# Optimization experiments

Hardware: AMD Instinct MI355X
Metric: run time of the kernel (lower is better)

## Reference

```python
import jax, jax.numpy as jnp
import numpy as np
from jax import lax

# program token ids
PAD, START, END, SCENE, INTERSECT, FILT, RELATE, QUERY = range(8)
SKIP = (PAD, START, END)


def conv2d(x, w, b, dil=1):
    # 'same' padding for odd kernels (3x3 pad=dil, 1x1 pad=0), NCHW/OIHW
    pad = dil * (w.shape[2] // 2)
    y = lax.conv_general_dilated(x, w, (1, 1), [(pad, pad), (pad, pad)],
                                 rhs_dilation=(dil, dil),
                                 dimension_numbers=('NCHW', 'OIHW', 'NCHW'))
    return y + b[None, :, None, None]


def maxpool2(x):
    return lax.reduce_window(x, -jnp.inf, lax.max, (1, 1, 2, 2), (1, 1, 2, 2), 'VALID')


def exec_program(prog, feat_input, p):
    """Run one (concrete) program over a batch of stem features. prog: tuple of ints,
    executed in reversed order exactly like TbDNet.forward."""
    B, _, H, W = feat_input.shape
    output = feat_input
    saved = None
    for t in reversed(prog):
        if t in SKIP:
            continue
        if t == SCENE:
            saved = output
            output = jnp.ones((B, 1, H, W), feat_input.dtype)
        elif t == INTERSECT:  # AndModule: elementwise min of attentions
            output = jnp.minimum(output, saved)
        elif t == FILT:
            a = feat_input * output  # [B,D,H,W] * [B,1,H,W]
            a = jax.nn.relu(conv2d(a, p['att_w1'], p['att_b1']))
            a = jax.nn.relu(conv2d(a, p['att_w2'], p['att_b2']))
            output = jax.nn.sigmoid(conv2d(a, p['att_w3'], p['att_b3']))
        elif t == RELATE:  # RelateModule: dilated conv stack (1,2,4,8,1) -> conv1x1 sigmoid
            a = feat_input * output
            for w, b, d in ((p['rel_w1'], p['rel_b1'], 1), (p['rel_w2'], p['rel_b2'], 2),
                            (p['rel_w3'], p['rel_b3'], 4), (p['rel_w4'], p['rel_b4'], 8),
                            (p['rel_w5'], p['rel_b5'], 1)):
                a = jax.nn.relu(conv2d(a, w, b, d))
            output = jax.nn.sigmoid(conv2d(a, p['rel_w6'], p['rel_b6']))
        elif t == QUERY:
            a = feat_input * output
            a = jax.nn.relu(conv2d(a, p['qry_w1'], p['qry_b1']))
            output = jax.nn.relu(conv2d(a, p['qry_w2'], p['qry_b2']))
    return output


def tbd_forward(feats, programs_np, p):
    B = feats.shape[0]
    stem = jax.nn.relu(conv2d(feats, p['stem_w1'], p['stem_b1']))
    stem = jax.nn.relu(conv2d(stem, p['stem_w2'], p['stem_b2']))  # [B,D,H,W]
    D, H, W = stem.shape[1], stem.shape[2], stem.shape[3]
    # group samples by identical program so dispatch runs batched, not per-sample
    groups = {}
    for n in range(B):
        groups.setdefault(tuple(int(v) for v in programs_np[n]), []).append(n)
    mod_out = jnp.zeros((B, D, H, W), feats.dtype)
    for prog, idxs in groups.items():
        idx = jnp.array(idxs)
        mod_out = mod_out.at[idx].set(exec_program(prog, stem[idx], p))
    # classifier: conv1x1 -> relu -> maxpool2 -> flatten -> fc -> relu -> fc
    x = jax.nn.relu(conv2d(mod_out, p['cls_w'], p['cls_b']))
    x = maxpool2(x)                        # [B,1024,7,7]
    x = x.reshape(B, -1)                   # [B,50176]
    x = jax.nn.relu(x @ p['fc1_w'].T + p['fc1_b'])
    return x @ p['fc2_w'].T + p['fc2_b']   # [B,28]


def setup_inputs() -> dict:
    key = jax.random.key(0)
    ks = iter(jax.random.split(key, 64))
    def rn(shape, s=0.05):
        return jax.random.normal(next(ks), shape, dtype=jnp.float32) * s
    B, Cin, H, W, D, P, L, A = 64, 1024, 14, 14, 128, 1024, 1024, 28
    feats = jax.random.normal(next(ks), (B, Cin, H, W), dtype=jnp.float32)
    # stored programs; execution order is reversed(stored)
    progA = [START, QUERY, FILT, RELATE, FILT, SCENE, END, PAD]            # scene->filter->relate->filter->query
    progB = [START, QUERY, INTERSECT, FILT, SCENE, FILT, SCENE, END]       # two filter branches -> intersect -> query
    programs = jnp.array([progA] * (B // 2) + [progB] * (B // 2), dtype=jnp.int32)
    inp = {'feats': feats, 'programs': programs,
           'stem_w1': rn((D, Cin, 3, 3), 0.02), 'stem_b1': rn((D,)),
           'stem_w2': rn((D, D, 3, 3)), 'stem_b2': rn((D,)),
           'att_w1': rn((D, D, 3, 3)), 'att_b1': rn((D,)),
           'att_w2': rn((D, D, 3, 3)), 'att_b2': rn((D,)),
           'att_w3': rn((1, D, 1, 1)), 'att_b3': rn((1,)),
           'rel_w1': rn((D, D, 3, 3)), 'rel_b1': rn((D,)),
           'rel_w2': rn((D, D, 3, 3)), 'rel_b2': rn((D,)),
           'rel_w3': rn((D, D, 3, 3)), 'rel_b3': rn((D,)),
           'rel_w4': rn((D, D, 3, 3)), 'rel_b4': rn((D,)),
           'rel_w5': rn((D, D, 3, 3)), 'rel_b5': rn((D,)),
           'rel_w6': rn((1, D, 1, 1)), 'rel_b6': rn((1,)),
           'qry_w1': rn((D, D, 3, 3)), 'qry_b1': rn((D,)),
           'qry_w2': rn((D, D, 3, 3)), 'qry_b2': rn((D,)),
           'cls_w': rn((P, D, 1, 1)), 'cls_b': rn((P,)),
           'fc1_w': rn((L, P * (H // 2) * (W // 2)), 0.01), 'fc1_b': rn((L,)),
           'fc2_w': rn((A, L)), 'fc2_b': rn((A,))}
    return inp


PARAM_NAMES = ['stem_w1', 'stem_b1', 'stem_w2', 'stem_b2',
               'att_w1', 'att_b1', 'att_w2', 'att_b2', 'att_w3', 'att_b3',
               'rel_w1', 'rel_b1', 'rel_w2', 'rel_b2', 'rel_w3', 'rel_b3',
               'rel_w4', 'rel_b4', 'rel_w5', 'rel_b5', 'rel_w6', 'rel_b6',
               'qry_w1', 'qry_b1', 'qry_w2', 'qry_b2',
               'cls_w', 'cls_b', 'fc1_w', 'fc1_b', 'fc2_w', 'fc2_b']


def reference(feats, programs, stem_w1, stem_b1, stem_w2, stem_b2,
              att_w1, att_b1, att_w2, att_b2, att_w3, att_b3,
              rel_w1, rel_b1, rel_w2, rel_b2, rel_w3, rel_b3,
              rel_w4, rel_b4, rel_w5, rel_b5, rel_w6, rel_b6,
              qry_w1, qry_b1, qry_w2, qry_b2,
              cls_w, cls_b, fc1_w, fc1_b, fc2_w, fc2_b):
    vals = [stem_w1, stem_b1, stem_w2, stem_b2,
            att_w1, att_b1, att_w2, att_b2, att_w3, att_b3,
            rel_w1, rel_b1, rel_w2, rel_b2, rel_w3, rel_b3,
            rel_w4, rel_b4, rel_w5, rel_b5, rel_w6, rel_b6,
            qry_w1, qry_b1, qry_w2, qry_b2,
            cls_w, cls_b, fc1_w, fc1_b, fc2_w, fc2_b]
    p = dict(zip(PARAM_NAMES, vals))
    return tbd_forward(feats, np.asarray(programs), p)
```

## Files before the change

kernel.cpp:

```cpp
#include <hip/hip_runtime.h>
#include <math.h>


typedef __attribute__((ext_vector_type(8)))  short   short8;
typedef __attribute__((ext_vector_type(8)))  __bf16  bf16x8;
typedef __attribute__((ext_vector_type(4)))  float   f32x4;

#define NROUNDS 15
#define NKS 49

#define B_WSTEM1 0UL
#define B_WSTEM2 2359296UL
#define B_WMOD   2654208UL
#define B_WCLS   5308416UL
#define B_STEM   5570560UL
#define B_XA     8781824UL
#define B_XB     11993088UL
#define B_FEAT   15204352UL
#define B_ATTN   18415616UL
#define B_SAVED  18465792UL
#define B_SCHED  18515968UL
#define B_ACTB   18520064UL
#define B_FC1T   24942592UL
#define B_S1P    B_XB
#define B_FC1P   B_STEM

__device__ __forceinline__ unsigned short f2bf(float f) {
    unsigned int b = __float_as_uint(f);
    b += 0x7fffu + ((b >> 16) & 1u);
    return (unsigned short)(b >> 16);
}
__device__ __forceinline__ float bf2f(unsigned short u) {
    return __uint_as_float(((unsigned int)u) << 16);
}
__device__ __forceinline__ f32x4 mfma16(bf16x8 a, bf16x8 b, f32x4 c) {
    return __builtin_amdgcn_mfma_f32_16x16x32_bf16(a, b, c, 0, 0, 0);
}

struct RepackArgs { const float* src[12]; };

__global__ __launch_bounds__(256) void k_repack(RepackArgs a, char* ws)
{
    const int y = blockIdx.y;
    const float* __restrict__ src = a.src[y];
    int gid = blockIdx.x * 256 + threadIdx.x;
    int gsz = gridDim.x * 256;
    if (y == 11) {
        unsigned short* dst = (unsigned short*)(ws + B_WCLS);
        for (int i = gid; i < 131072; i += gsz) dst[i] = f2bf(src[i]);
    } else {
        const int IC = (y == 0) ? 1024 : 128;
        const int lg = (y == 0) ? 10 : 7;
        unsigned short* dst = (unsigned short*)(ws + ((y == 0) ? B_WSTEM1
                                    : (y == 1) ? B_WSTEM2
                                    : B_WMOD + (size_t)(y - 2) * 294912));
        const int total = 9 << (lg + 7);
        for (int i = gid; i < total; i += gsz) {
            int ic = i & (IC - 1);
            int oc = (i >> lg) & 127;
            int t  = i >> (lg + 7);
            dst[i] = f2bf(src[((size_t)oc * IC + ic) * 9 + t]);
        }
    }
}

__global__ __launch_bounds__(256) void k_decode_init(const int* __restrict__ prog, char* ws)
{
    int gid = blockIdx.x * 256 + threadIdx.x;
    int gsz = gridDim.x * 256;
    float* attn  = (float*)(ws + B_ATTN);
    float* saved = (float*)(ws + B_SAVED);
    for (int i = gid; i < 64 * 196; i += gsz) { attn[i] = 1.0f; saved[i] = 1.0f; }
    unsigned int* fz = (unsigned int*)(ws + B_FEAT);
    for (int i = gid; i < 64 * 25088 / 2; i += gsz) fz[i] = 0u;
    if (gid < 64) {
        int n = gid;
        int ent[NROUNDS];
        for (int r = 0; r < NROUNDS; ++r) ent[r] = 0;
        int rc = 0;
#define ENC(op,wv,dl,g,s,d) ((op)|((wv)<<4)|((dl)<<8)|((g)<<12)|((s)<<13)|((d)<<15))
#define EMIT(v) do { if (rc < NROUNDS) ent[rc++] = (v); } while (0)
        for (int j = 7; j >= 0; --j) {
            int t = prog[n * 8 + j];
            switch (t) {
                case 3: EMIT(ENC(1,0,0,0,0,0)); break;
                case 4: EMIT(ENC(2,0,0,0,0,0)); break;
                case 5:
                    EMIT(ENC(3,0,1,1,3,0));
                    EMIT(ENC(3,1,1,0,0,1));
                    EMIT(ENC(4,0,0,0,1,0));
                    break;
                case 6:
                    EMIT(ENC(3,2,1,1,3,0));
                    EMIT(ENC(3,3,2,0,0,1));
                    EMIT(ENC(3,4,4,0,1,0));
                    EMIT(ENC(3,5,8,0,0,1));
                    EMIT(ENC(3,6,1,0,1,0));
                    EMIT(ENC(4,1,0,0,0,0));
                    break;
                case 7:
                    EMIT(ENC(3,7,1,1,3,0));
                    EMIT(ENC(3,8,1,0,0,2));
                    break;
                default: break;
            }
        }
#undef EMIT
#undef ENC
        int* sched = (int*)(ws + B_SCHED);
        for (int r = 0; r < NROUNDS; ++r) sched[n * NROUNDS + r] = ent[r];
    }
}

__global__ __launch_bounds__(256) void k_stem1p(const float* __restrict__ feats,
                                                const unsigned short* __restrict__ wrep,
                                                char* ws)
{
    __shared__ unsigned short s_img[197 * 136];
    const int bx = blockIdx.x;
    const int n = bx >> 4, ks = (bx >> 2) & 3, och = (bx >> 1) & 1, pxh = bx & 1;
    const int tid = threadIdx.x, lane = tid & 63;
    const int w = tid >> 6, wm = w & 1, wn = w >> 1;
    const int l15 = lane & 15, lq = lane >> 4;

    if (tid < 68) ((unsigned int*)s_img)[196 * 68 + tid] = 0u;

    int pglob[4], pbyt[4], pyv[4], pxv[4];
#pragma unroll
    for (int j = 0; j < 4; ++j) {
        int nt = wn + 2 * j;
        int p  = (pxh * 7 + nt) * 16 + l15;
        pglob[j] = p;
        int py = p / 14;
        pyv[j] = (p < 196) ? py : 10000;
        pxv[j] = p - py * 14;
        pbyt[j] = p * 272 + lq * 16;
    }
    const int zaddr = 196 * 272 + lq * 16;
    const int nNT = (wn == 0) ? 4 : 3;

    f32x4 acc[2][4];
#pragma unroll
    for (int m = 0; m < 2; ++m)
#pragma unroll
        for (int j = 0; j < 4; ++j) acc[m][j] = (f32x4){0.f, 0.f, 0.f, 0.f};

    const int icg = tid & 31;

    for (int slab = 0; slab < 2; ++slab) {
        if (slab) __syncthreads();
        const int icb = ks * 256 + slab * 128;
        const float* sf = feats + ((size_t)n * 1024 + icb) * 196;
        for (int qq = (tid >> 5); qq < 49; qq += 8) {
            const float* p0 = sf + icg * 4 * 196 + qq * 4;
            float4 r0 = *(const float4*)(p0);
            float4 r1 = *(const float4*)(p0 + 196);
            float4 r2 = *(const float4*)(p0 + 392);
            float4 r3 = *(const float4*)(p0 + 588);
#pragma unroll
            for (int e = 0; e < 4; ++e) {
                uint2 v;
                v.x = (unsigned int)f2bf(((const float*)&r0)[e]) |
                      ((unsigned int)f2bf(((const float*)&r1)[e]) << 16);
                v.y = (unsigned int)f2bf(((const float*)&r2)[e]) |
                      ((unsigned int)f2bf(((const float*)&r3)[e]) << 16);
                *(uint2*)(s_img + (qq * 4 + e) * 136 + icg * 4) = v;
            }
        }
        __syncthreads();

#pragma unroll
        for (int t = 0; t < 9; ++t) {
            const int dy = t / 3 - 1, dx = t % 3 - 1;
            int baddr[4];
#pragma unroll
            for (int j = 0; j < 4; ++j) {
                int yy = pyv[j] + dy, xx = pxv[j] + dx;
                bool ok = ((unsigned)yy < 14u) && ((unsigned)xx < 14u);
                baddr[j] = ok ? (pbyt[j] + (dy * 14 + dx) * 272) : zaddr;
            }
#pragma unroll
            for (int kc = 0; kc < 4; ++kc) {
                const unsigned short* wt = wrep +
                    ((size_t)(t * 128 + och * 64 + wm * 32 + l15) * 1024 + icb + kc * 32 + lq * 8);
                bf16x8 a0 = *(const bf16x8*)(wt);
                bf16x8 a1 = *(const bf16x8*)(wt + 16 * 1024);
#pragma unroll
                for (int j = 0; j < 4; ++j) {
                    if (j < nNT) {
                        bf16x8 b = *(const bf16x8*)((const char*)s_img + baddr[j] + kc * 64);
                        acc[0][j] = mfma16(a0, b, acc[0][j]);
                        acc[1][j] = mfma16(a1, b, acc[1][j]);
                    }
                }
            }
        }
    }

    unsigned short* part = (unsigned short*)(ws + B_S1P);
#pragma unroll
    for (int m = 0; m < 2; ++m) {
        const int oc = och * 64 + wm * 32 + m * 16 + lq * 4;
#pragma unroll
        for (int j = 0; j < 4; ++j) {
            if (j < nNT) {
                int p = pglob[j];
                if (p < 196) {
                    unsigned int lo = (unsigned int)f2bf(acc[m][j][0]) |
                                      ((unsigned int)f2bf(acc[m][j][1]) << 16);
                    unsigned int hi = (unsigned int)f2bf(acc[m][j][2]) |
                                      ((unsigned int)f2bf(acc[m][j][3]) << 16);
                    uint2 pk; pk.x = lo; pk.y = hi;
                    *(uint2*)(part + (((size_t)ks * 64 + n) * 196 + p) * 128 + oc) = pk;
                }
            }
        }
    }
}

__global__ __launch_bounds__(256) void k_stem1r(const char* __restrict__ ws_c,
                                                const float* __restrict__ bias,
                                                unsigned short* __restrict__ xa)
{
    int i = blockIdx.x * 256 + threadIdx.x;
    const unsigned short* part = (const unsigned short*)(ws_c + B_S1P);
    int oc8 = (i & 15) * 8;
    int np  = i >> 4;
    float s[8] = {};
#pragma unroll
    for (int ks = 0; ks < 4; ++ks) {
        short8 v = *(const short8*)(part + (((size_t)ks * 64) * 196 + np) * 128 + oc8);
#pragma unroll
        for (int e = 0; e < 8; ++e) s[e] += bf2f((unsigned short)v[e]);
    }
    short8 o;
#pragma unroll
    for (int e = 0; e < 8; ++e)
        o[e] = (short)f2bf(fmaxf(s[e] + bias[oc8 + e], 0.f));
    *(short8*)(xa + (size_t)np * 128 + oc8) = o;
}

__device__ void conv_mfma_core(const unsigned short* __restrict__ srcB,
                               const float*  __restrict__ gate,
                               const unsigned short* __restrict__ wrep,
                               const float*  __restrict__ bias,
                               unsigned short* __restrict__ dst,
                               int dil, int och, int pxh,
                               unsigned short* s_img)
{
    const int tid  = threadIdx.x, lane = tid & 63;
    const int w    = tid >> 6, wm = w & 1, wn = w >> 1;
    const int l15  = lane & 15, lq = lane >> 4;

    if (tid < 68) ((unsigned int*)s_img)[196 * 68 + tid] = 0u;

    int pglob[4], pbyt[4], pyv[4], pxv[4];
#pragma unroll
    for (int j = 0; j < 4; ++j) {
        int nt = wn + 2 * j;
        int p  = (pxh * 7 + nt) * 16 + l15;
        pglob[j] = p;
        int py = p / 14;
        pyv[j] = (p < 196) ? py : 10000;
        pxv[j] = p - py * 14;
        pbyt[j] = p * 272 + lq * 16;
    }
    const int zaddr = 196 * 272 + lq * 16;
    const int nNT = (wn == 0) ? 4 : 3;

    f32x4 acc[2][4];
#pragma unroll
    for (int m = 0; m < 2; ++m)
#pragma unroll
        for (int j = 0; j < 4; ++j) acc[m][j] = (f32x4){0.f, 0.f, 0.f, 0.f};

    if (gate) {
        for (int i = tid; i < 196 * 16; i += 256) {
            int p = i >> 4, c8 = (i & 15) * 8;
            short8 v = *(const short8*)(srcB + p * 128 + c8);
            float g = gate[p];
            short8 ov;
#pragma unroll
            for (int e = 0; e < 8; ++e)
                ov[e] = (short)f2bf(bf2f((unsigned short)v[e]) * g);
            *(short8*)(s_img + p * 136 + c8) = ov;
        }
    } else {
        for (int i = tid; i < 196 * 16; i += 256) {
            int p = i >> 4, c8 = (i & 15) * 8;
            *(short8*)(s_img + p * 136 + c8) = *(const short8*)(srcB + p * 128 + c8);
        }
    }
    __syncthreads();

    const unsigned short* wlane = wrep + (size_t)(och * 64 + wm * 32 + l15) * 128 + lq * 8;
#pragma unroll
    for (int t = 0; t < 9; ++t) {
        const int dy = (t / 3 - 1) * dil, dx = (t % 3 - 1) * dil;
        int baddr[4];
#pragma unroll
        for (int j = 0; j < 4; ++j) {
            int yy = pyv[j] + dy, xx = pxv[j] + dx;
            bool ok = ((unsigned)yy < 14u) && ((unsigned)xx < 14u);
            baddr[j] = ok ? (pbyt[j] + (dy * 14 + dx) * 272) : zaddr;
        }
        const unsigned short* wt = wlane + (size_t)(t * 128) * 128;
#pragma unroll
        for (int kc = 0; kc < 4; ++kc) {
            bf16x8 a0 = *(const bf16x8*)(wt + kc * 32);
            bf16x8 a1 = *(const bf16x8*)(wt + (size_t)16 * 128 + kc * 32);
#pragma unroll
            for (int j = 0; j < 4; ++j) {
                if (j < nNT) {
                    bf16x8 b = *(const bf16x8*)((const char*)s_img + baddr[j] + kc * 64);
                    acc[0][j] = mfma16(a0, b, acc[0][j]);
                    acc[1][j] = mfma16(a1, b, acc[1][j]);
                }
            }
        }
    }

#pragma unroll
    for (int m = 0; m < 2; ++m) {
        const int oc = och * 64 + wm * 32 + m * 16 + lq * 4;
        const float4 b4 = *(const float4*)(bias + oc);
#pragma unroll
        for (int j = 0; j < 4; ++j) {
            if (j < nNT) {
                int p = pglob[j];
                if (p < 196) {
                    float v0 = fmaxf(acc[m][j][0] + b4.x, 0.f);
                    float v1 = fmaxf(acc[m][j][1] + b4.y, 0.f);
                    float v2 = fmaxf(acc[m][j][2] + b4.z, 0.f);
                    float v3 = fmaxf(acc[m][j][3] + b4.w, 0.f);
                    unsigned int lo = (unsigned int)f2bf(v0) | ((unsigned int)f2bf(v1) << 16);
                    unsigned int hi = (unsigned int)f2bf(v2) | ((unsigned int)f2bf(v3) << 16);
                    uint2 pk; pk.x = lo; pk.y = hi;
                    *(uint2*)(dst + p * 128 + oc) = pk;
                }
            }
        }
    }
}

__global__ __launch_bounds__(256) void k_conv_stem2(const unsigned short* __restrict__ srcBall,
                                                    const unsigned short* __restrict__ wrep,
                                                    const float* __restrict__ bias,
                                                    unsigned short* __restrict__ dstall)
{
    __shared__ unsigned short s_img[197 * 136];
    const int n = blockIdx.x >> 2, och = (blockIdx.x >> 1) & 1, pxh = blockIdx.x & 1;
    conv_mfma_core(srcBall + (size_t)n * 25088, nullptr, wrep, bias,
                   dstall + (size_t)n * 25088, 1, och, pxh, s_img);
}

struct RArgs {
    char* ws;
    const float* mbias[9];
    const float* w1x1[2];
    const float* b1x1[2];
};

__global__ __launch_bounds__(256) void k_round(RArgs a, int r)
{
    __shared__ unsigned short s_img[197 * 136];
    const int bx = blockIdx.x;
    const int n = bx >> 2, och = (bx >> 1) & 1, pxh = bx & 1;
    char* ws = a.ws;
    const int* sched = (const int*)(ws + B_SCHED);
    const int e = sched[n * NROUNDS + r];
    const int op = e & 15;
    if (op == 0) return;
    float* attn  = (float*)(ws + B_ATTN)  + n * 196;
    float* saved = (float*)(ws + B_SAVED) + n * 196;
    if (op == 1 || op == 2) {
        if ((bx & 3) == 0 && threadIdx.x < 196) {
            int p = threadIdx.x;
            if (op == 1) { saved[p] = attn[p]; attn[p] = 1.0f; }
            else         attn[p] = fminf(attn[p], saved[p]);
        }
        return;
    }
    const int wset = (e >> 4) & 15, dil = (e >> 8) & 15, gatef = (e >> 12) & 1;
    const int srcid = (e >> 13) & 3, dstid = (e >> 15) & 3;
    const unsigned short* src = (const unsigned short*)(ws +
            (srcid == 3 ? B_STEM : srcid == 1 ? B_XB : B_XA)) + (size_t)n * 25088;
    if (op == 4) {
        if ((bx & 3) == 0 && threadIdx.x < 196) {
            int p = threadIdx.x;
            const float* wv = a.w1x1[wset];
            float acc = a.b1x1[wset][0];
            const unsigned short* row = src + p * 128;
#pragma unroll 8
            for (int ic = 0; ic < 128; ++ic) acc += bf2f(row[ic]) * wv[ic];
            attn[p] = 1.0f / (1.0f + __expf(-acc));
        }
        return;
    }
    unsigned short* dst = (unsigned short*)(ws +
            (dstid == 2 ? B_FEAT : dstid == 1 ? B_XB : B_XA)) + (size_t)n * 25088;
    const unsigned short* wrep = (const unsigned short*)(ws + B_WMOD) + (size_t)wset * 9 * 128 * 128;
    conv_mfma_core(src, gatef ? attn : nullptr, wrep, a.mbias[wset], dst,
                   dil, och, pxh, s_img);
}

__global__ __launch_bounds__(256) void k_cls_pool(const unsigned short* __restrict__ featall,
                                                  const unsigned short* __restrict__ clsw,
                                                  const float* __restrict__ clsb,
                                                  unsigned short* __restrict__ actB)
{
    __shared__ char smem[197 * 272 + 64 * 200 * 4];
    unsigned short* s_img = (unsigned short*)smem;
    float* s_pool = (float*)(smem + 197 * 272);
    const int n = blockIdx.x >> 4, pt = blockIdx.x & 15;
    const int tid = threadIdx.x, lane = tid & 63, w = tid >> 6;
    const int l15 = lane & 15, lq = lane >> 4;
    const unsigned short* feat = featall + (size_t)n * 25088;

    if (tid < 68) ((unsigned int*)s_img)[196 * 68 + tid] = 0u;
    for (int i = tid; i < 196 * 16; i += 256) {
        int p = i >> 4, c8 = (i & 15) * 8;
        *(short8*)(s_img + p * 136 + c8) = *(const short8*)(feat + p * 128 + c8);
    }
    f32x4 acc[14];
#pragma unroll
    for (int j = 0; j < 14; ++j) acc[j] = (f32x4){0.f, 0.f, 0.f, 0.f};
    __syncthreads();

    const unsigned short* wl = clsw + (size_t)(pt * 64 + w * 16 + l15) * 128 + lq * 8;
#pragma unroll
    for (int kc = 0; kc < 4; ++kc) {
        bf16x8 a0 = *(const bf16x8*)(wl + kc * 32);
#pragma unroll
        for (int j = 0; j < 14; ++j) {
            int p = j * 16 + l15;
            int ba = (p < 196) ? (p * 272 + lq * 16 + kc * 64) : (196 * 272 + lq * 16);
            bf16x8 b = *(const bf16x8*)((const char*)s_img + ba);
            acc[j] = mfma16(a0, b, acc[j]);
        }
    }
    const int oc = pt * 64 + w * 16 + lq * 4;
    const float4 b4 = *(const float4*)(clsb + oc);
    const int pl = w * 16 + lq * 4;
#pragma unroll
    for (int j = 0; j < 14; ++j) {
        int p = j * 16 + l15;
        if (p < 196) {
            s_pool[(pl + 0) * 200 + p] = fmaxf(acc[j][0] + b4.x, 0.f);
            s_pool[(pl + 1) * 200 + p] = fmaxf(acc[j][1] + b4.y, 0.f);
            s_pool[(pl + 2) * 200 + p] = fmaxf(acc[j][2] + b4.z, 0.f);
            s_pool[(pl + 3) * 200 + p] = fmaxf(acc[j][3] + b4.w, 0.f);
        }
    }
    __syncthreads();
    for (int i = tid; i < 64 * 49; i += 256) {
        int plx = i / 49, q = i - plx * 49;
        int py = q / 7, qx = q - py * 7;
        const float* rp = s_pool + plx * 200 + py * 28 + qx * 2;
        float m = fmaxf(fmaxf(rp[0], rp[1]), fmaxf(rp[14], rp[15]));
        int k = (pt * 64 + plx) * 49 + q;
        int kb = k >> 6, lq2 = (k >> 4) & 3, hi = (k >> 3) & 1, e = k & 7;
        actB[((((size_t)kb * 4 + lq2) * 2 + hi) * 64 + n) * 8 + e] = f2bf(m);
    }
}

__global__ __launch_bounds__(256) void k_fc1p(const unsigned short* __restrict__ actB,
                                              const float* __restrict__ w,
                                              float* __restrict__ part)
{
    __shared__ unsigned short s_w[64 * 264];
    const int jt = blockIdx.x & 15, ks = blockIdx.x >> 4;
    const int tid = threadIdx.x, lane = tid & 63, wv = tid >> 6;
    const int l15 = lane & 15, lq = lane >> 4;
    const int k0 = ks * 1024;
    const int r4 = tid & 3, l4 = (tid >> 2) & 15, rw = tid >> 6;

    f32x4 acc[4];
#pragma unroll
    for (int t = 0; t < 4; ++t) acc[t] = (f32x4){0.f, 0.f, 0.f, 0.f};

    float4 pf[4][4];

#define FC1_LOAD(ss_) do {                                                        \
    _Pragma("unroll")                                                             \
    for (int pass = 0; pass < 4; ++pass) {                                        \
        const int row_ = pass * 16 + rw * 4 + r4;                                 \
        const float* wp_ = w + (size_t)(jt * 64 + row_) * 50176 + k0              \
                             + (ss_) * 256 + l4 * 16;                             \
        pf[pass][0] = *(const float4*)(wp_);                                      \
        pf[pass][1] = *(const float4*)(wp_ + 4);                                  \
        pf[pass][2] = *(const float4*)(wp_ + 8);                                  \
        pf[pass][3] = *(const float4*)(wp_ + 12);                                 \
    } } while (0)

    FC1_LOAD(0);

    for (int ss = 0; ss < 4; ++ss) {
        __syncthreads();
#pragma unroll
        for (int pass = 0; pass < 4; ++pass) {
            const int row = pass * 16 + rw * 4 + r4;
            bf16x8 c0, c1;
            c0[0] = (__bf16)pf[pass][0].x; c0[1] = (__bf16)pf[pass][0].y;
            c0[2] = (__bf16)pf[pass][0].z; c0[3] = (__bf16)pf[pass][0].w;
            c0[4] = (__bf16)pf[pass][1].x; c0[5] = (__bf16)pf[pass][1].y;
            c0[6] = (__bf16)pf[pass][1].z; c0[7] = (__bf16)pf[pass][1].w;
            c1[0] = (__bf16)pf[pass][2].x; c1[1] = (__bf16)pf[pass][2].y;
            c1[2] = (__bf16)pf[pass][2].z; c1[3] = (__bf16)pf[pass][2].w;
            c1[4] = (__bf16)pf[pass][3].x; c1[5] = (__bf16)pf[pass][3].y;
            c1[6] = (__bf16)pf[pass][3].z; c1[7] = (__bf16)pf[pass][3].w;
            *(bf16x8*)(s_w + row * 264 + l4 * 16)     = c0;
            *(bf16x8*)(s_w + row * 264 + l4 * 16 + 8) = c1;
        }
        __syncthreads();
        if (ss < 3) FC1_LOAD(ss + 1);

        const unsigned short* arow = s_w + (wv * 16 + l15) * 264;
#pragma unroll
        for (int kk = 0; kk < 8; ++kk) {
            bf16x8 a = *(const bf16x8*)(arow + kk * 32 + lq * 8);
            const int kglob = k0 + ss * 256 + kk * 32 + lq * 8;
            const int kb = kglob >> 6, lq2 = (kglob >> 4) & 3, hi = (kglob >> 3) & 1;
            const unsigned short* bp = actB +
                ((((size_t)kb * 4 + lq2) * 2 + hi) * 64 + l15) * 8;
#pragma unroll
            for (int t = 0; t < 4; ++t) {
                bf16x8 b = *(const bf16x8*)(bp + t * 128);
                acc[t] = mfma16(a, b, acc[t]);
            }
        }
    }
#undef FC1_LOAD

    float* pbase = part + ((size_t)ks * 1024 + jt * 64 + wv * 16 + lq * 4) * 64 + l15;
#pragma unroll
    for (int t = 0; t < 4; ++t)
#pragma unroll
        for (int r = 0; r < 4; ++r)
            pbase[(size_t)r * 64 + t * 16] = acc[t][r];
}

__global__ __launch_bounds__(256) void k_fc1r(const float* __restrict__ part,
                                              const float* __restrict__ b,
                                              float* __restrict__ fc1T)
{
    int i = blockIdx.x * 256 + threadIdx.x;
    if (i >= 65536) return;
    float s = 0.0f;
    for (int ks = 0; ks < NKS; ++ks) s += part[(size_t)ks * 65536 + i];
    int j = i >> 6;
    fc1T[i] = fmaxf(s + b[j], 0.0f);
}

__global__ __launch_bounds__(256) void k_fc2(const float* __restrict__ fc1T,
                                             const float* __restrict__ w,
                                             const float* __restrict__ b,
                                             float* __restrict__ out)
{
    __shared__ float red[256];
    const int a_ = blockIdx.x;
    const int tid = threadIdx.x, lane = tid & 63, q = tid >> 6;
    float acc = 0.0f;
    const float* wr = w + (size_t)a_ * 1024;
    for (int k = q * 256; k < q * 256 + 256; ++k)
        acc = fmaf(fc1T[k * 64 + lane], wr[k], acc);
    red[tid] = acc;
    __syncthreads();
    if (q == 0) {
        float s = red[tid] + red[tid + 64] + red[tid + 128] + red[tid + 192] + b[a_];
        out[lane * 28 + a_] = s;
    }
}

extern "C" void kernel_launch(void* const* d_in, const int* in_sizes, int n_in,
                              void* d_out, int out_size, void* d_ws, size_t ws_size,
                              hipStream_t stream)
{
    const float* feats = (const float*)d_in[0];
    const int*   prog  = (const int*)d_in[1];
    char* ws  = (char*)d_ws;
    float* out = (float*)d_out;

    RepackArgs ra;
    ra.src[0]  = (const float*)d_in[2];
    ra.src[1]  = (const float*)d_in[4];
    ra.src[2]  = (const float*)d_in[6];
    ra.src[3]  = (const float*)d_in[8];
    ra.src[4]  = (const float*)d_in[12];
    ra.src[5]  = (const float*)d_in[14];
    ra.src[6]  = (const float*)d_in[16];
    ra.src[7]  = (const float*)d_in[18];
    ra.src[8]  = (const float*)d_in[20];
    ra.src[9]  = (const float*)d_in[24];
    ra.src[10] = (const float*)d_in[26];
    ra.src[11] = (const float*)d_in[28];

    k_repack<<<dim3(64, 12), 256, 0, stream>>>(ra, ws);

    k_stem1p<<<1024, 256, 0, stream>>>(feats, (const unsigned short*)(ws + B_WSTEM1), ws);
    k_stem1r<<<784, 256, 0, stream>>>(ws, (const float*)d_in[3],
                                      (unsigned short*)(ws + B_XA));

    k_decode_init<<<256, 256, 0, stream>>>(prog, ws);

    k_conv_stem2<<<256, 256, 0, stream>>>((const unsigned short*)(ws + B_XA),
                                          (const unsigned short*)(ws + B_WSTEM2),
                                          (const float*)d_in[5],
                                          (unsigned short*)(ws + B_STEM));

    RArgs ga;
    ga.ws = ws;
    ga.mbias[0] = (const float*)d_in[7];
    ga.mbias[1] = (const float*)d_in[9];
    ga.mbias[2] = (const float*)d_in[13];
    ga.mbias[3] = (const float*)d_in[15];
    ga.mbias[4] = (const float*)d_in[17];
    ga.mbias[5] = (const float*)d_in[19];
    ga.mbias[6] = (const float*)d_in[21];
    ga.mbias[7] = (const float*)d_in[25];
    ga.mbias[8] = (const float*)d_in[27];
    ga.w1x1[0]  = (const float*)d_in[10];
    ga.w1x1[1]  = (const float*)d_in[22];
    ga.b1x1[0]  = (const float*)d_in[11];
    ga.b1x1[1]  = (const float*)d_in[23];

    for (int r = 0; r < NROUNDS; ++r)
        k_round<<<256, 256, 0, stream>>>(ga, r);

    k_cls_pool<<<1024, 256, 0, stream>>>((const unsigned short*)(ws + B_FEAT),
                                         (const unsigned short*)(ws + B_WCLS),
                                         (const float*)d_in[29],
                                         (unsigned short*)(ws + B_ACTB));
    k_fc1p<<<784, 256, 0, stream>>>((const unsigned short*)(ws + B_ACTB),
                                    (const float*)d_in[30], (float*)(ws + B_FC1P));
    k_fc1r<<<256, 256, 0, stream>>>((const float*)(ws + B_FC1P), (const float*)d_in[31],
                                    (float*)(ws + B_FC1T));
    k_fc2<<<28, 256, 0, stream>>>((const float*)(ws + B_FC1T), (const float*)d_in[32],
                                  (const float*)d_in[33], out);
}
```

Baseline: 598.9 us.

## Fuse stem2 and all program rounds into one persistent per-sample LDS kernel

Replaces the stem2 conv kernel and the 15 per-round launches with a single kernel that has one 512-thread block per sample. Activations, attention and saved maps stay in LDS across all rounds, and only the final output goes to global memory. Each block now computes all 128 output channels and all pixels, and stem1p is reshaped the same way (256 blocks of 512 threads instead of 1024 of 256). This removes launch overhead and global round-trips between rounds, but only 64 blocks run on a GPU with many more CUs, which cuts parallelism and uses about 160KB of LDS per block.

```diff
diff --git a/kernel.cpp b/kernel.cpp
--- a/kernel.cpp
+++ b/kernel.cpp
@@ -24,6 +24,14 @@
 #define B_FC1T   24942592UL
 #define B_S1P    B_XB
 #define B_FC1P   B_STEM
+
+#define PC_BUF0  0
+#define PC_BUF1  53312
+#define PC_BUF2  106624
+#define PC_ZERO  159936
+#define PC_ATTN  160208
+#define PC_SAVED 160992
+#define PC_TOTAL 161776
 
 __device__ __forceinline__ unsigned short f2bf(float f) {
     unsigned int b = __float_as_uint(f);
@@ -68,9 +76,6 @@
 {
     int gid = blockIdx.x * 256 + threadIdx.x;
     int gsz = gridDim.x * 256;
-    float* attn  = (float*)(ws + B_ATTN);
-    float* saved = (float*)(ws + B_SAVED);
-    for (int i = gid; i < 64 * 196; i += gsz) { attn[i] = 1.0f; saved[i] = 1.0f; }
     unsigned int* fz = (unsigned int*)(ws + B_FEAT);
     for (int i = gid; i < 64 * 25088 / 2; i += gsz) fz[i] = 0u;
     if (gid < 64) {
@@ -86,12 +91,12 @@
                 case 3: EMIT(ENC(1,0,0,0,0,0)); break;
                 case 4: EMIT(ENC(2,0,0,0,0,0)); break;
                 case 5:
-                    EMIT(ENC(3,0,1,1,3,0));
+                    EMIT(ENC(3,0,1,1,2,0));
                     EMIT(ENC(3,1,1,0,0,1));
                     EMIT(ENC(4,0,0,0,1,0));
                     break;
                 case 6:
-                    EMIT(ENC(3,2,1,1,3,0));
+                    EMIT(ENC(3,2,1,1,2,0));
                     EMIT(ENC(3,3,2,0,0,1));
                     EMIT(ENC(3,4,4,0,1,0));
                     EMIT(ENC(3,5,8,0,0,1));
@@ -99,8 +104,8 @@
                     EMIT(ENC(4,1,0,0,0,0));
                     break;
                 case 7:
-                    EMIT(ENC(3,7,1,1,3,0));
-                    EMIT(ENC(3,8,1,0,0,2));
+                    EMIT(ENC(3,7,1,1,2,0));
+                    EMIT(ENC(3,8,1,0,0,3));
                     break;
                 default: break;
             }
@@ -112,13 +117,13 @@
     }
 }
 
-__global__ __launch_bounds__(256) void k_stem1p(const float* __restrict__ feats,
+__global__ __launch_bounds__(512) void k_stem1p(const float* __restrict__ feats,
                                                 const unsigned short* __restrict__ wrep,
                                                 char* ws)
 {
     __shared__ unsigned short s_img[197 * 136];
     const int bx = blockIdx.x;
-    const int n = bx >> 4, ks = (bx >> 2) & 3, och = (bx >> 1) & 1, pxh = bx & 1;
+    const int n = bx >> 2, ks = bx & 3;
     const int tid = threadIdx.x, lane = tid & 63;
     const int w = tid >> 6, wm = w & 1, wn = w >> 1;
     const int l15 = lane & 15, lq = lane >> 4;
@@ -128,8 +133,7 @@
     int pglob[4], pbyt[4], pyv[4], pxv[4];
 #pragma unroll
     for (int j = 0; j < 4; ++j) {
-        int nt = wn + 2 * j;
-        int p  = (pxh * 7 + nt) * 16 + l15;
+        int p  = (wn + 4 * j) * 16 + l15;
         pglob[j] = p;
         int py = p / 14;
         pyv[j] = (p < 196) ? py : 10000;
@@ -137,21 +141,22 @@
         pbyt[j] = p * 272 + lq * 16;
     }
     const int zaddr = 196 * 272 + lq * 16;
-    const int nNT = (wn == 0) ? 4 : 3;
-
-    f32x4 acc[2][4];
-#pragma unroll
-    for (int m = 0; m < 2; ++m)
+    const int nJ = (wn == 0) ? 4 : 3;
+
+    f32x4 acc[4][4];
+#pragma unroll
+    for (int m = 0; m < 4; ++m)
 #pragma unroll
         for (int j = 0; j < 4; ++j) acc[m][j] = (f32x4){0.f, 0.f, 0.f, 0.f};
 
     const int icg = tid & 31;
+    const int qq0 = tid >> 5;
 
     for (int slab = 0; slab < 2; ++slab) {
         if (slab) __syncthreads();
         const int icb = ks * 256 + slab * 128;
         const float* sf = feats + ((size_t)n * 1024 + icb) * 196;
-        for (int qq = (tid >> 5); qq < 49; qq += 8) {
+        for (int qq = qq0; qq < 49; qq += 16) {
             const float* p0 = sf + icg * 4 * 196 + qq * 4;
             float4 r0 = *(const float4*)(p0);
             float4 r1 = *(const float4*)(p0 + 196);
@@ -182,15 +187,18 @@
 #pragma unroll
             for (int kc = 0; kc < 4; ++kc) {
                 const unsigned short* wt = wrep +
-                    ((size_t)(t * 128 + och * 64 + wm * 32 + l15) * 1024 + icb + kc * 32 + lq * 8);
-                bf16x8 a0 = *(const bf16x8*)(wt);
-                bf16x8 a1 = *(const bf16x8*)(wt + 16 * 1024);
+                    ((size_t)(t * 128 + wm * 64 + l15) * 1024 + icb + kc * 32 + lq * 8);
+                bf16x8 am[4];
+#pragma unroll
+                for (int m = 0; m < 4; ++m)
+                    am[m] = *(const bf16x8*)(wt + (size_t)m * 16 * 1024);
 #pragma unroll
                 for (int j = 0; j < 4; ++j) {
-                    if (j < nNT) {
+                    if (j < nJ) {
                         bf16x8 b = *(const bf16x8*)((const char*)s_img + baddr[j] + kc * 64);
-                        acc[0][j] = mfma16(a0, b, acc[0][j]);
-                        acc[1][j] = mfma16(a1, b, acc[1][j]);
+#pragma unroll
+                        for (int m = 0; m < 4; ++m)
+                            acc[m][j] = mfma16(am[m], b, acc[m][j]);
                     }
                 }
             }
@@ -199,11 +207,11 @@
 
     unsigned short* part = (unsigned short*)(ws + B_S1P);
 #pragma unroll
-    for (int m = 0; m < 2; ++m) {
-        const int oc = och * 64 + wm * 32 + m * 16 + lq * 4;
+    for (int m = 0; m < 4; ++m) {
+        const int oc = wm * 64 + m * 16 + lq * 4;
 #pragma unroll
         for (int j = 0; j < 4; ++j) {
-            if (j < nNT) {
+            if (j < nJ) {
                 int p = pglob[j];
                 if (p < 196) {
                     unsigned int lo = (unsigned int)f2bf(acc[m][j][0]) |
@@ -240,60 +248,50 @@
     *(short8*)(xa + (size_t)np * 128 + oc8) = o;
 }
 
-__device__ void conv_mfma_core(const unsigned short* __restrict__ srcB,
-                               const float*  __restrict__ gate,
-                               const unsigned short* __restrict__ wrep,
-                               const float*  __restrict__ bias,
-                               unsigned short* __restrict__ dst,
-                               int dil, int och, int pxh,
-                               unsigned short* s_img)
-{
-    const int tid  = threadIdx.x, lane = tid & 63;
-    const int w    = tid >> 6, wm = w & 1, wn = w >> 1;
-    const int l15  = lane & 15, lq = lane >> 4;
-
-    if (tid < 68) ((unsigned int*)s_img)[196 * 68 + tid] = 0u;
+__device__ void prog_conv(char* sm, int srcoff, int dstoff,
+                          unsigned short* gdst,
+                          const unsigned short* __restrict__ wrep,
+                          const float* __restrict__ bias,
+                          int dil, int gated, const float* s_attn)
+{
+    const int tid = threadIdx.x, lane = tid & 63;
+    const int w = tid >> 6, wm = w & 1, wn = w >> 1;
+    const int l15 = lane & 15, lq = lane >> 4;
+
+    if (gated) {
+        for (int i = tid; i < 196 * 16; i += 512) {
+            int p = i >> 4, c8 = (i & 15) * 8;
+            short8 v = *(const short8*)(sm + srcoff + p * 272 + c8 * 2);
+            float g = s_attn[p];
+            short8 ov;
+#pragma unroll
+            for (int e = 0; e < 8; ++e)
+                ov[e] = (short)f2bf(bf2f((unsigned short)v[e]) * g);
+            *(short8*)(sm + dstoff + p * 272 + c8 * 2) = ov;
+        }
+        srcoff = dstoff;
+    }
+    __syncthreads();
 
     int pglob[4], pbyt[4], pyv[4], pxv[4];
 #pragma unroll
     for (int j = 0; j < 4; ++j) {
-        int nt = wn + 2 * j;
-        int p  = (pxh * 7 + nt) * 16 + l15;
+        int p  = (wn + 4 * j) * 16 + l15;
         pglob[j] = p;
         int py = p / 14;
         pyv[j] = (p < 196) ? py : 10000;
         pxv[j] = p - py * 14;
-        pbyt[j] = p * 272 + lq * 16;
-    }
-    const int zaddr = 196 * 272 + lq * 16;
-    const int nNT = (wn == 0) ? 4 : 3;
-
-    f32x4 acc[2][4];
-#pragma unroll
-    for (int m = 0; m < 2; ++m)
+        pbyt[j] = srcoff + p * 272 + lq * 16;
+    }
+    const int zaddr = PC_ZERO + lq * 16;
+    const int nJ = (wn == 0) ? 4 : 3;
+
+    f32x4 acc[4][4];
+#pragma unroll
+    for (int m = 0; m < 4; ++m)
 #pragma unroll
         for (int j = 0; j < 4; ++j) acc[m][j] = (f32x4){0.f, 0.f, 0.f, 0.f};
 
-    if (gate) {
-        for (int i = tid; i < 196 * 16; i += 256) {
-            int p = i >> 4, c8 = (i & 15) * 8;
-            short8 v = *(const short8*)(srcB + p * 128 + c8);
-            float g = gate[p];
-            short8 ov;
-#pragma unroll
-            for (int e = 0; e < 8; ++e)
-                ov[e] = (short)f2bf(bf2f((unsigned short)v[e]) * g);
-            *(short8*)(s_img + p * 136 + c8) = ov;
-        }
-    } else {
-        for (int i = tid; i < 196 * 16; i += 256) {
-            int p = i >> 4, c8 = (i & 15) * 8;
-            *(short8*)(s_img + p * 136 + c8) = *(const short8*)(srcB + p * 128 + c8);
-        }
-    }
-    __syncthreads();
-
-    const unsigned short* wlane = wrep + (size_t)(och * 64 + wm * 32 + l15) * 128 + lq * 8;
 #pragma unroll
     for (int t = 0; t < 9; ++t) {
         const int dy = (t / 3 - 1) * dil, dx = (t % 3 - 1) * dil;
@@ -304,104 +302,129 @@
             bool ok = ((unsigned)yy < 14u) && ((unsigned)xx < 14u);
             baddr[j] = ok ? (pbyt[j] + (dy * 14 + dx) * 272) : zaddr;
         }
-        const unsigned short* wt = wlane + (size_t)(t * 128) * 128;
 #pragma unroll
         for (int kc = 0; kc < 4; ++kc) {
-            bf16x8 a0 = *(const bf16x8*)(wt + kc * 32);
-            bf16x8 a1 = *(const bf16x8*)(wt + (size_t)16 * 128 + kc * 32);
+            const unsigned short* wt = wrep +
+                ((size_t)(t * 128 + wm * 64 + l15) * 128 + kc * 32 + lq * 8);
+            bf16x8 am[4];
+#pragma unroll
+            for (int m = 0; m < 4; ++m)
+                am[m] = *(const bf16x8*)(wt + (size_t)m * 16 * 128);
 #pragma unroll
             for (int j = 0; j < 4; ++j) {
-                if (j < nNT) {
-                    bf16x8 b = *(const bf16x8*)((const char*)s_img + baddr[j] + kc * 64);
-                    acc[0][j] = mfma16(a0, b, acc[0][j]);
-                    acc[1][j] = mfma16(a1, b, acc[1][j]);
+                if (j < nJ) {
+                    bf16x8 b = *(const bf16x8*)(sm + baddr[j] + kc * 64);
+#pragma unroll
+                    for (int m = 0; m < 4; ++m)
+                        acc[m][j] = mfma16(am[m], b, acc[m][j]);
                 }
             }
         }
     }
-
-#pragma unroll
-    for (int m = 0; m < 2; ++m) {
-        const int oc = och * 64 + wm * 32 + m * 16 + lq * 4;
+    __syncthreads();
+
+#pragma unroll
+    for (int m = 0; m < 4; ++m) {
+        const int oc = wm * 64 + m * 16 + lq * 4;
         const float4 b4 = *(const float4*)(bias + oc);
 #pragma unroll
         for (int j = 0; j < 4; ++j) {
-            if (j < nNT) {
+            if (j < nJ) {
                 int p = pglob[j];
                 if (p < 196) {
                     float v0 = fmaxf(acc[m][j][0] + b4.x, 0.f);
                     float v1 = fmaxf(acc[m][j][1] + b4.y, 0.f);
                     float v2 = fmaxf(acc[m][j][2] + b4.z, 0.f);
                     float v3 = fmaxf(acc[m][j][3] + b4.w, 0.f);
-                    unsigned int lo = (unsigned int)f2bf(v0) | ((unsigned int)f2bf(v1) << 16);
-                    unsigned int hi = (unsigned int)f2bf(v2) | ((unsigned int)f2bf(v3) << 16);
-                    uint2 pk; pk.x = lo; pk.y = hi;
-                    *(uint2*)(dst + p * 128 + oc) = pk;
+                    uint2 pk;
+                    pk.x = (unsigned int)f2bf(v0) | ((unsigned int)f2bf(v1) << 16);
+                    pk.y = (unsigned int)f2bf(v2) | ((unsigned int)f2bf(v3) << 16);
+                    if (gdst) *(uint2*)(gdst + p * 128 + oc) = pk;
+                    else      *(uint2*)(sm + dstoff + p * 272 + oc * 2) = pk;
                 }
             }
         }
     }
-}
-
-__global__ __launch_bounds__(256) void k_conv_stem2(const unsigned short* __restrict__ srcBall,
-                                                    const unsigned short* __restrict__ wrep,
-                                                    const float* __restrict__ bias,
-                                                    unsigned short* __restrict__ dstall)
-{
-    __shared__ unsigned short s_img[197 * 136];
-    const int n = blockIdx.x >> 2, och = (blockIdx.x >> 1) & 1, pxh = blockIdx.x & 1;
-    conv_mfma_core(srcBall + (size_t)n * 25088, nullptr, wrep, bias,
-                   dstall + (size_t)n * 25088, 1, och, pxh, s_img);
-}
-
-struct RArgs {
+    __syncthreads();
+}
+
+struct PArgs {
     char* ws;
+    const unsigned short* xa;
+    unsigned short* feat;
+    const float* stem2b;
     const float* mbias[9];
     const float* w1x1[2];
     const float* b1x1[2];
 };
 
-__global__ __launch_bounds__(256) void k_round(RArgs a, int r)
-{
-    __shared__ unsigned short s_img[197 * 136];
-    const int bx = blockIdx.x;
-    const int n = bx >> 2, och = (bx >> 1) & 1, pxh = bx & 1;
-    char* ws = a.ws;
-    const int* sched = (const int*)(ws + B_SCHED);
-    const int e = sched[n * NROUNDS + r];
-    const int op = e & 15;
-    if (op == 0) return;
-    float* attn  = (float*)(ws + B_ATTN)  + n * 196;
-    float* saved = (float*)(ws + B_SAVED) + n * 196;
-    if (op == 1 || op == 2) {
-        if ((bx & 3) == 0 && threadIdx.x < 196) {
-            int p = threadIdx.x;
-            if (op == 1) { saved[p] = attn[p]; attn[p] = 1.0f; }
-            else         attn[p] = fminf(attn[p], saved[p]);
-        }
-        return;
-    }
-    const int wset = (e >> 4) & 15, dil = (e >> 8) & 15, gatef = (e >> 12) & 1;
-    const int srcid = (e >> 13) & 3, dstid = (e >> 15) & 3;
-    const unsigned short* src = (const unsigned short*)(ws +
-            (srcid == 3 ? B_STEM : srcid == 1 ? B_XB : B_XA)) + (size_t)n * 25088;
-    if (op == 4) {
-        if ((bx & 3) == 0 && threadIdx.x < 196) {
-            int p = threadIdx.x;
-            const float* wv = a.w1x1[wset];
-            float acc = a.b1x1[wset][0];
-            const unsigned short* row = src + p * 128;
-#pragma unroll 8
-            for (int ic = 0; ic < 128; ++ic) acc += bf2f(row[ic]) * wv[ic];
-            attn[p] = 1.0f / (1.0f + __expf(-acc));
-        }
-        return;
-    }
-    unsigned short* dst = (unsigned short*)(ws +
-            (dstid == 2 ? B_FEAT : dstid == 1 ? B_XB : B_XA)) + (size_t)n * 25088;
-    const unsigned short* wrep = (const unsigned short*)(ws + B_WMOD) + (size_t)wset * 9 * 128 * 128;
-    conv_mfma_core(src, gatef ? attn : nullptr, wrep, a.mbias[wset], dst,
-                   dil, och, pxh, s_img);
+__global__ __launch_bounds__(512) void k_prog(PArgs a)
+{
+    __shared__ char sm[PC_TOTAL];
+    const int n = blockIdx.x;
+    const int tid = threadIdx.x;
+    float* s_attn  = (float*)(sm + PC_ATTN);
+    float* s_saved = (float*)(sm + PC_SAVED);
+
+    if (tid < 68) ((unsigned int*)(sm + PC_ZERO))[tid] = 0u;
+    if (tid < 196) { s_attn[tid] = 1.0f; s_saved[tid] = 1.0f; }
+    {
+        const unsigned short* xa = a.xa + (size_t)n * 25088;
+        for (int i = tid; i < 196 * 16; i += 512) {
+            int p = i >> 4, c8 = (i & 15) * 8;
+            *(short8*)(sm + PC_BUF0 + p * 272 + c8 * 2) = *(const short8*)(xa + p * 128 + c8);
+        }
+    }
+    __syncthreads();
+
+    const unsigned short* wstem2 = (const unsigned short*)(a.ws + B_WSTEM2);
+    const unsigned short* wmod   = (const unsigned short*)(a.ws + B_WMOD);
+    const int* sched = (const int*)(a.ws + B_SCHED);
+
+    prog_conv(sm, PC_BUF0, PC_BUF2, nullptr, wstem2, a.stem2b, 1, 0, s_attn);
+
+    for (int r = 0; r < NROUNDS; ++r) {
+        const int e = sched[n * NROUNDS + r];
+        const int op = e & 15;
+        if (op == 0) continue;
+        if (op == 1) {
+            if (tid < 196) { s_saved[tid] = s_attn[tid]; s_attn[tid] = 1.0f; }
+            __syncthreads();
+            continue;
+        }
+        if (op == 2) {
+            if (tid < 196) s_attn[tid] = fminf(s_attn[tid], s_saved[tid]);
+            __syncthreads();
+            continue;
+        }
+        const int wset = (e >> 4) & 15, dil = (e >> 8) & 15, g = (e >> 12) & 1;
+        const int si = (e >> 13) & 3, di = (e >> 15) & 3;
+        const int so = (si == 2) ? PC_BUF2 : (si == 1) ? PC_BUF1 : PC_BUF0;
+        if (op == 4) {
+            if (tid < 196) {
+                const float* wv = a.w1x1[wset];
+                float accv = a.b1x1[wset][0];
+                const char* row = sm + so + tid * 272;
+#pragma unroll
+                for (int c = 0; c < 16; ++c) {
+                    short8 v = *(const short8*)(row + c * 16);
+#pragma unroll
+                    for (int e2 = 0; e2 < 8; ++e2)
+                        accv += bf2f((unsigned short)v[e2]) * wv[c * 8 + e2];
+                }
+                s_attn[tid] = 1.0f / (1.0f + __expf(-accv));
+            }
+            __syncthreads();
+            continue;
+        }
+        unsigned short* gd = nullptr;
+        int dof = PC_BUF0;
+        if (di == 3)      gd  = a.feat + (size_t)n * 25088;
+        else if (di == 2) dof = PC_BUF2;
+        else if (di == 1) dof = PC_BUF1;
+        prog_conv(sm, so, dof, gd, wmod + (size_t)wset * 147456,
+                  a.mbias[wset], dil, g, s_attn);
+    }
 }
 
 __global__ __launch_bounds__(256) void k_cls_pool(const unsigned short* __restrict__ featall,
@@ -597,35 +620,32 @@
 
     k_repack<<<dim3(64, 12), 256, 0, stream>>>(ra, ws);
 
-    k_stem1p<<<1024, 256, 0, stream>>>(feats, (const unsigned short*)(ws + B_WSTEM1), ws);
+    k_stem1p<<<256, 512, 0, stream>>>(feats, (const unsigned short*)(ws + B_WSTEM1), ws);
     k_stem1r<<<784, 256, 0, stream>>>(ws, (const float*)d_in[3],
                                       (unsigned short*)(ws + B_XA));
 
     k_decode_init<<<256, 256, 0, stream>>>(prog, ws);
 
-    k_conv_stem2<<<256, 256, 0, stream>>>((const unsigned short*)(ws + B_XA),
-                                          (const unsigned short*)(ws + B_WSTEM2),
-                                          (const float*)d_in[5],
-                                          (unsigned short*)(ws + B_STEM));
-
-    RArgs ga;
-    ga.ws = ws;
-    ga.mbias[0] = (const float*)d_in[7];
-    ga.mbias[1] = (const float*)d_in[9];
-    ga.mbias[2] = (const float*)d_in[13];
-    ga.mbias[3] = (const float*)d_in[15];
-    ga.mbias[4] = (const float*)d_in[17];
-    ga.mbias[5] = (const float*)d_in[19];
-    ga.mbias[6] = (const float*)d_in[21];
-    ga.mbias[7] = (const float*)d_in[25];
-    ga.mbias[8] = (const float*)d_in[27];
-    ga.w1x1[0]  = (const float*)d_in[10];
-    ga.w1x1[1]  = (const float*)d_in[22];
-    ga.b1x1[0]  = (const float*)d_in[11];
-    ga.b1x1[1]  = (const float*)d_in[23];
-
-    for (int r = 0; r < NROUNDS; ++r)
-        k_round<<<256, 256, 0, stream>>>(ga, r);
+    PArgs pa;
+    pa.ws = ws;
+    pa.xa = (const unsigned short*)(ws + B_XA);
+    pa.feat = (unsigned short*)(ws + B_FEAT);
+    pa.stem2b = (const float*)d_in[5];
+    pa.mbias[0] = (const float*)d_in[7];
+    pa.mbias[1] = (const float*)d_in[9];
+    pa.mbias[2] = (const float*)d_in[13];
+    pa.mbias[3] = (const float*)d_in[15];
+    pa.mbias[4] = (const float*)d_in[17];
+    pa.mbias[5] = (const float*)d_in[19];
+    pa.mbias[6] = (const float*)d_in[21];
+    pa.mbias[7] = (const float*)d_in[25];
+    pa.mbias[8] = (const float*)d_in[27];
+    pa.w1x1[0]  = (const float*)d_in[10];
+    pa.w1x1[1]  = (const float*)d_in[22];
+    pa.b1x1[0]  = (const float*)d_in[11];
+    pa.b1x1[1]  = (const float*)d_in[23];
+
+    k_prog<<<64, 512, 0, stream>>>(pa);
 
     k_cls_pool<<<1024, 256, 0, stream>>>((const unsigned short*)(ws + B_FEAT),
                                          (const unsigned short*)(ws + B_WCLS),
```

New measurement: 703.0 us. +17.4%, slower.

## Rebalance work split: fuse stem1 tiles per block, halve conv output-channel tile

Applied to the files above, without the earlier changes.

The stem1 partial kernel now runs 512-thread blocks, one per (image, K-slice). Each block computes all 128 output channels and all pixel tiles, so the fp32-to-bf16 image staging is done once instead of four times. The shared 3x3 conv core (stem2 and the 15 per-round module kernels) now splits output channels into four 32-channel tiles instead of two 64-channel ones, doubling the grid to 512 blocks. This gives more parallelism on the many-CU device, at the cost of staging the gated input image into LDS twice as often per image. Stem1 also carries more accumulators per thread, which raises register pressure.

```diff
diff --git a/kernel.cpp b/kernel.cpp
--- a/kernel.cpp
+++ b/kernel.cpp
@@ -112,13 +112,13 @@
     }
 }
 
-__global__ __launch_bounds__(256) void k_stem1p(const float* __restrict__ feats,
+__global__ __launch_bounds__(512) void k_stem1p(const float* __restrict__ feats,
                                                 const unsigned short* __restrict__ wrep,
                                                 char* ws)
 {
     __shared__ unsigned short s_img[197 * 136];
     const int bx = blockIdx.x;
-    const int n = bx >> 4, ks = (bx >> 2) & 3, och = (bx >> 1) & 1, pxh = bx & 1;
+    const int n = bx >> 2, ks = bx & 3;
     const int tid = threadIdx.x, lane = tid & 63;
     const int w = tid >> 6, wm = w & 1, wn = w >> 1;
     const int l15 = lane & 15, lq = lane >> 4;
@@ -128,8 +128,7 @@
     int pglob[4], pbyt[4], pyv[4], pxv[4];
 #pragma unroll
     for (int j = 0; j < 4; ++j) {
-        int nt = wn + 2 * j;
-        int p  = (pxh * 7 + nt) * 16 + l15;
+        int p  = (wn + 4 * j) * 16 + l15;
         pglob[j] = p;
         int py = p / 14;
         pyv[j] = (p < 196) ? py : 10000;
@@ -137,21 +136,22 @@
         pbyt[j] = p * 272 + lq * 16;
     }
     const int zaddr = 196 * 272 + lq * 16;
-    const int nNT = (wn == 0) ? 4 : 3;
-
-    f32x4 acc[2][4];
-#pragma unroll
-    for (int m = 0; m < 2; ++m)
+    const int nJ = (wn == 0) ? 4 : 3;
+
+    f32x4 acc[4][4];
+#pragma unroll
+    for (int m = 0; m < 4; ++m)
 #pragma unroll
         for (int j = 0; j < 4; ++j) acc[m][j] = (f32x4){0.f, 0.f, 0.f, 0.f};
 
     const int icg = tid & 31;
+    const int qq0 = tid >> 5;
 
     for (int slab = 0; slab < 2; ++slab) {
         if (slab) __syncthreads();
         const int icb = ks * 256 + slab * 128;
         const float* sf = feats + ((size_t)n * 1024 + icb) * 196;
-        for (int qq = (tid >> 5); qq < 49; qq += 8) {
+        for (int qq = qq0; qq < 49; qq += 16) {
             const float* p0 = sf + icg * 4 * 196 + qq * 4;
             float4 r0 = *(const float4*)(p0);
             float4 r1 = *(const float4*)(p0 + 196);
@@ -182,15 +182,18 @@
 #pragma unroll
             for (int kc = 0; kc < 4; ++kc) {
                 const unsigned short* wt = wrep +
-                    ((size_t)(t * 128 + och * 64 + wm * 32 + l15) * 1024 + icb + kc * 32 + lq * 8);
-                bf16x8 a0 = *(const bf16x8*)(wt);
-                bf16x8 a1 = *(const bf16x8*)(wt + 16 * 1024);
+                    ((size_t)(t * 128 + wm * 64 + l15) * 1024 + icb + kc * 32 + lq * 8);
+                bf16x8 am[4];
+#pragma unroll
+                for (int m = 0; m < 4; ++m)
+                    am[m] = *(const bf16x8*)(wt + (size_t)m * 16 * 1024);
 #pragma unroll
                 for (int j = 0; j < 4; ++j) {
-                    if (j < nNT) {
+                    if (j < nJ) {
                         bf16x8 b = *(const bf16x8*)((const char*)s_img + baddr[j] + kc * 64);
-                        acc[0][j] = mfma16(a0, b, acc[0][j]);
-                        acc[1][j] = mfma16(a1, b, acc[1][j]);
+#pragma unroll
+                        for (int m = 0; m < 4; ++m)
+                            acc[m][j] = mfma16(am[m], b, acc[m][j]);
                     }
                 }
             }
@@ -199,11 +202,11 @@
 
     unsigned short* part = (unsigned short*)(ws + B_S1P);
 #pragma unroll
-    for (int m = 0; m < 2; ++m) {
-        const int oc = och * 64 + wm * 32 + m * 16 + lq * 4;
+    for (int m = 0; m < 4; ++m) {
+        const int oc = wm * 64 + m * 16 + lq * 4;
 #pragma unroll
         for (int j = 0; j < 4; ++j) {
-            if (j < nNT) {
+            if (j < nJ) {
                 int p = pglob[j];
                 if (p < 196) {
                     unsigned int lo = (unsigned int)f2bf(acc[m][j][0]) |
@@ -245,7 +248,7 @@
                                const unsigned short* __restrict__ wrep,
                                const float*  __restrict__ bias,
                                unsigned short* __restrict__ dst,
-                               int dil, int och, int pxh,
+                               int dil, int oct, int pxh,
                                unsigned short* s_img)
 {
     const int tid  = threadIdx.x, lane = tid & 63;
@@ -268,11 +271,9 @@
     const int zaddr = 196 * 272 + lq * 16;
     const int nNT = (wn == 0) ? 4 : 3;
 
-    f32x4 acc[2][4];
-#pragma unroll
-    for (int m = 0; m < 2; ++m)
-#pragma unroll
-        for (int j = 0; j < 4; ++j) acc[m][j] = (f32x4){0.f, 0.f, 0.f, 0.f};
+    f32x4 acc[4];
+#pragma unroll
+    for (int j = 0; j < 4; ++j) acc[j] = (f32x4){0.f, 0.f, 0.f, 0.f};
 
     if (gate) {
         for (int i = tid; i < 196 * 16; i += 256) {
@@ -293,7 +294,7 @@
     }
     __syncthreads();
 
-    const unsigned short* wlane = wrep + (size_t)(och * 64 + wm * 32 + l15) * 128 + lq * 8;
+    const unsigned short* wlane = wrep + (size_t)(oct * 32 + wm * 16 + l15) * 128 + lq * 8;
 #pragma unroll
     for (int t = 0; t < 9; ++t) {
         const int dy = (t / 3 - 1) * dil, dx = (t % 3 - 1) * dil;
@@ -308,36 +309,31 @@
 #pragma unroll
         for (int kc = 0; kc < 4; ++kc) {
             bf16x8 a0 = *(const bf16x8*)(wt + kc * 32);
-            bf16x8 a1 = *(const bf16x8*)(wt + (size_t)16 * 128 + kc * 32);
 #pragma unroll
             for (int j = 0; j < 4; ++j) {
                 if (j < nNT) {
                     bf16x8 b = *(const bf16x8*)((const char*)s_img + baddr[j] + kc * 64);
-                    acc[0][j] = mfma16(a0, b, acc[0][j]);
-                    acc[1][j] = mfma16(a1, b, acc[1][j]);
+                    acc[j] = mfma16(a0, b, acc[j]);
                 }
             }
         }
     }
 
-#pragma unroll
-    for (int m = 0; m < 2; ++m) {
-        const int oc = och * 64 + wm * 32 + m * 16 + lq * 4;
-        const float4 b4 = *(const float4*)(bias + oc);
-#pragma unroll
-        for (int j = 0; j < 4; ++j) {
-            if (j < nNT) {
-                int p = pglob[j];
-                if (p < 196) {
-                    float v0 = fmaxf(acc[m][j][0] + b4.x, 0.f);
-                    float v1 = fmaxf(acc[m][j][1] + b4.y, 0.f);
-                    float v2 = fmaxf(acc[m][j][2] + b4.z, 0.f);
-                    float v3 = fmaxf(acc[m][j][3] + b4.w, 0.f);
-                    unsigned int lo = (unsigned int)f2bf(v0) | ((unsigned int)f2bf(v1) << 16);
-                    unsigned int hi = (unsigned int)f2bf(v2) | ((unsigned int)f2bf(v3) << 16);
-                    uint2 pk; pk.x = lo; pk.y = hi;
-                    *(uint2*)(dst + p * 128 + oc) = pk;
-                }
+    const int oc = oct * 32 + wm * 16 + lq * 4;
+    const float4 b4 = *(const float4*)(bias + oc);
+#pragma unroll
+    for (int j = 0; j < 4; ++j) {
+        if (j < nNT) {
+            int p = pglob[j];
+            if (p < 196) {
+                float v0 = fmaxf(acc[j][0] + b4.x, 0.f);
+                float v1 = fmaxf(acc[j][1] + b4.y, 0.f);
+                float v2 = fmaxf(acc[j][2] + b4.z, 0.f);
+                float v3 = fmaxf(acc[j][3] + b4.w, 0.f);
+                uint2 pk;
+                pk.x = (unsigned int)f2bf(v0) | ((unsigned int)f2bf(v1) << 16);
+                pk.y = (unsigned int)f2bf(v2) | ((unsigned int)f2bf(v3) << 16);
+                *(uint2*)(dst + p * 128 + oc) = pk;
             }
         }
     }
@@ -349,9 +345,9 @@
                                                     unsigned short* __restrict__ dstall)
 {
     __shared__ unsigned short s_img[197 * 136];
-    const int n = blockIdx.x >> 2, och = (blockIdx.x >> 1) & 1, pxh = blockIdx.x & 1;
+    const int n = blockIdx.x >> 3, oct = (blockIdx.x >> 1) & 3, pxh = blockIdx.x & 1;
     conv_mfma_core(srcBall + (size_t)n * 25088, nullptr, wrep, bias,
-                   dstall + (size_t)n * 25088, 1, och, pxh, s_img);
+                   dstall + (size_t)n * 25088, 1, oct, pxh, s_img);
 }
 
 struct RArgs {
@@ -365,7 +361,7 @@
 {
     __shared__ unsigned short s_img[197 * 136];
     const int bx = blockIdx.x;
-    const int n = bx >> 2, och = (bx >> 1) & 1, pxh = bx & 1;
+    const int n = bx >> 3, oct = (bx >> 1) & 3, pxh = bx & 1;
     char* ws = a.ws;
     const int* sched = (const int*)(ws + B_SCHED);
     const int e = sched[n * NROUNDS + r];
@@ -374,7 +370,7 @@
     float* attn  = (float*)(ws + B_ATTN)  + n * 196;
     float* saved = (float*)(ws + B_SAVED) + n * 196;
     if (op == 1 || op == 2) {
-        if ((bx & 3) == 0 && threadIdx.x < 196) {
+        if ((bx & 7) == 0 && threadIdx.x < 196) {
             int p = threadIdx.x;
             if (op == 1) { saved[p] = attn[p]; attn[p] = 1.0f; }
             else         attn[p] = fminf(attn[p], saved[p]);
@@ -386,7 +382,7 @@
     const unsigned short* src = (const unsigned short*)(ws +
             (srcid == 3 ? B_STEM : srcid == 1 ? B_XB : B_XA)) + (size_t)n * 25088;
     if (op == 4) {
-        if ((bx & 3) == 0 && threadIdx.x < 196) {
+        if ((bx & 7) == 0 && threadIdx.x < 196) {
             int p = threadIdx.x;
             const float* wv = a.w1x1[wset];
             float acc = a.b1x1[wset][0];
@@ -401,7 +397,7 @@
             (dstid == 2 ? B_FEAT : dstid == 1 ? B_XB : B_XA)) + (size_t)n * 25088;
     const unsigned short* wrep = (const unsigned short*)(ws + B_WMOD) + (size_t)wset * 9 * 128 * 128;
     conv_mfma_core(src, gatef ? attn : nullptr, wrep, a.mbias[wset], dst,
-                   dil, och, pxh, s_img);
+                   dil, oct, pxh, s_img);
 }
 
 __global__ __launch_bounds__(256) void k_cls_pool(const unsigned short* __restrict__ featall,
@@ -597,13 +593,13 @@
 
     k_repack<<<dim3(64, 12), 256, 0, stream>>>(ra, ws);
 
-    k_stem1p<<<1024, 256, 0, stream>>>(feats, (const unsigned short*)(ws + B_WSTEM1), ws);
+    k_stem1p<<<256, 512, 0, stream>>>(feats, (const unsigned short*)(ws + B_WSTEM1), ws);
     k_stem1r<<<784, 256, 0, stream>>>(ws, (const float*)d_in[3],
                                       (unsigned short*)(ws + B_XA));
 
     k_decode_init<<<256, 256, 0, stream>>>(prog, ws);
 
-    k_conv_stem2<<<256, 256, 0, stream>>>((const unsigned short*)(ws + B_XA),
+    k_conv_stem2<<<512, 256, 0, stream>>>((const unsigned short*)(ws + B_XA),
                                           (const unsigned short*)(ws + B_WSTEM2),
                                           (const float*)d_in[5],
                                           (unsigned short*)(ws + B_STEM));
@@ -625,7 +621,7 @@
     ga.b1x1[1]  = (const float*)d_in[23];
 
     for (int r = 0; r < NROUNDS; ++r)
-        k_round<<<256, 256, 0, stream>>>(ga, r);
+        k_round<<<512, 256, 0, stream>>>(ga, r);
 
     k_cls_pool<<<1024, 256, 0, stream>>>((const unsigned short*)(ws + B_FEAT),
                                          (const unsigned short*)(ws + B_WCLS),
```

After: 546.1 us. 8.8% less time.
